# Optimization experiments

Measured on AMD Instinct MI355X. Metric: run time of the kernel, lower is better.

## Reference

```python
import jax, jax.numpy as jnp
import numpy as np

N_NODES = 100000
N_EDGES = 3200000
N_REL = 32
DIM = 64


def setup_inputs() -> dict:
    key = jax.random.key(0)
    ks = jax.random.split(key, 12)
    inp = {
        "ego_embeddings": jax.random.normal(ks[0], (N_NODES, DIM), dtype=jnp.float32),
        "rel_embeddings": jax.random.normal(ks[1], (N_REL, DIM), dtype=jnp.float32),
        "row_idx": jax.random.randint(ks[2], (N_EDGES,), 0, N_NODES, dtype=jnp.int32),
        "col_idx": jax.random.randint(ks[3], (N_EDGES,), 0, N_NODES, dtype=jnp.int32),
        "vals": jax.random.uniform(ks[4], (N_EDGES,), dtype=jnp.float32),
        "row_idx_r": jax.random.randint(ks[5], (N_EDGES,), 0, N_NODES, dtype=jnp.int32),
        "rel_idx": jax.random.randint(ks[6], (N_EDGES,), 0, N_REL, dtype=jnp.int32),
        "vals_r": jax.random.uniform(ks[7], (N_EDGES,), dtype=jnp.float32),
        "W1": jax.random.normal(ks[8], (DIM, DIM), dtype=jnp.float32) / np.sqrt(DIM),
        "b1": jnp.zeros((DIM,), dtype=jnp.float32),
        "W2": jax.random.normal(ks[9], (DIM, DIM), dtype=jnp.float32) / np.sqrt(DIM),
        "b2": jnp.zeros((DIM,), dtype=jnp.float32),
    }
    return inp


def _spmm(row, col, val, dense, num_rows):
    # sparse [num_rows, K] (COO) @ dense [K, D] -> [num_rows, D]
    msgs = val[:, None] * dense[col]  # [E, D]
    return jax.ops.segment_sum(msgs, row, num_segments=num_rows)


def reference(ego_embeddings, rel_embeddings, row_idx, col_idx, vals,
              row_idx_r, rel_idx, vals_r, W1, b1, W2, b2):
    n = ego_embeddings.shape[0]
    side = _spmm(row_idx, col_idx, vals, ego_embeddings, n) \
         + 0.1 * _spmm(row_idx_r, rel_idx, vals_r, rel_embeddings, n)
    # 'bi' aggregator
    add_emb = ego_embeddings + side
    sum_emb = jax.nn.leaky_relu(add_emb @ W1.T + b1, negative_slope=0.01)
    bi_emb = jax.nn.leaky_relu((ego_embeddings * side) @ W2.T + b2, negative_slope=0.01)
    # message dropout: identity in eval mode
    return bi_emb + sum_emb
```

## Files before the change

### kernel.cpp

```cpp
#include <hip/hip_runtime.h>
#include <hip/hip_fp16.h>

#define NN 100000
#define NE 3200000
#define NR 32
#define DIM 64
#define SCAN_BLK 1024
#define NBLK_SCAN ((NN + SCAN_BLK - 1) / SCAN_BLK)


__global__ __launch_bounds__(256) void hist_kernel(
    const int* __restrict__ row,
    const int* __restrict__ row_r, const int* __restrict__ rel_i,
    const float* __restrict__ vals_r,
    int* __restrict__ offsets, float* __restrict__ coeff)
{
    int e = blockIdx.x * 256 + threadIdx.x;
    if (e >= NE) return;
    atomicAdd(&offsets[row[e]], 1);
    atomicAdd(&coeff[row_r[e] * NR + rel_i[e]], vals_r[e]);
}

__global__ __launch_bounds__(SCAN_BLK) void scan1_kernel(
    int* __restrict__ offsets, int* __restrict__ bsums)
{
    __shared__ int s[SCAN_BLK];
    int tid = threadIdx.x;
    int i = blockIdx.x * SCAN_BLK + tid;
    int v = (i < NN) ? offsets[i] : 0;
    s[tid] = v;
    __syncthreads();
    for (int off = 1; off < SCAN_BLK; off <<= 1) {
        int t = (tid >= off) ? s[tid - off] : 0;
        __syncthreads();
        s[tid] += t;
        __syncthreads();
    }
    if (i < NN) offsets[i] = s[tid] - v;
    if (tid == SCAN_BLK - 1) bsums[blockIdx.x] = s[tid];
}

__global__ __launch_bounds__(128) void scan2_kernel(int* __restrict__ bsums)
{
    __shared__ int s[128];
    int tid = threadIdx.x;
    int v = (tid < NBLK_SCAN) ? bsums[tid] : 0;
    s[tid] = v;
    __syncthreads();
    for (int off = 1; off < 128; off <<= 1) {
        int t = (tid >= off) ? s[tid - off] : 0;
        __syncthreads();
        s[tid] += t;
        __syncthreads();
    }
    if (tid < NBLK_SCAN) bsums[tid] = s[tid] - v;
}

__global__ __launch_bounds__(SCAN_BLK) void scan3_kernel(
    int* __restrict__ offsets, const int* __restrict__ bsums)
{
    int i = blockIdx.x * SCAN_BLK + threadIdx.x;
    if (i < NN) offsets[i] += bsums[blockIdx.x];
}

__global__ __launch_bounds__(256) void scatter_kernel(
    const int* __restrict__ row, const int* __restrict__ col,
    const float* __restrict__ vals,
    int* __restrict__ offsets, int* __restrict__ ecol, __half* __restrict__ eval)
{
    int e = blockIdx.x * 256 + threadIdx.x;
    if (e >= NE) return;
    int pos = atomicAdd(&offsets[row[e]], 1);
    ecol[pos] = col[e];
    eval[pos] = __float2half(vals[e]);
}

__global__ __launch_bounds__(256) void gather_finalize_kernel(
    const float* __restrict__ ego, const float* __restrict__ rel_emb,
    const int* __restrict__ offsets, const int* __restrict__ ecol,
    const __half* __restrict__ eval, const float* __restrict__ coeff,
    const float* __restrict__ W1, const float* __restrict__ b1,
    const float* __restrict__ W2, const float* __restrict__ b2,
    float* __restrict__ out)
{
    __shared__ float sW1t[DIM * DIM];
    __shared__ float sW2t[DIM * DIM];
    __shared__ float sRel[NR * DIM];

    for (int i = threadIdx.x; i < DIM * DIM; i += 256) {
        int dd = i >> 6, kk = i & 63;
        sW1t[kk * DIM + dd] = W1[i];
        sW2t[kk * DIM + dd] = W2[i];
    }
    for (int i = threadIdx.x; i < NR * DIM; i += 256) sRel[i] = rel_emb[i];
    __syncthreads();

    const int wave = threadIdx.x >> 6;
    const int lane = threadIdx.x & 63;
    const int NPW  = 4;
    int node0 = (blockIdx.x * 4 + wave) * NPW;

    float bb1 = b1[lane];
    float bb2 = b2[lane];

    for (int t = 0; t < NPW; ++t) {
        int n = node0 + t;
        if (n >= NN) return;

        int start = (n > 0) ? offsets[n - 1] : 0;
        int end   = offsets[n];

        float acc = 0.0f;
        for (int base = start; base < end; base += 64) {
            int idx = base + lane;
            int   c = 0;
            float v = 0.0f;
            if (idx < end) { c = ecol[idx]; v = __half2float(eval[idx]); }
            int m = min(64, end - base);
            for (int j = 0; j < m; ++j) {
                int   cc = __shfl(c, j, 64);
                float vv = __shfl(v, j, 64);
                acc += vv * ego[cc * DIM + lane];
            }
        }

        float cv = (lane < NR) ? coeff[n * NR + lane] : 0.0f;
        float rp = 0.0f;
        #pragma unroll
        for (int r = 0; r < NR; ++r) {
            float c = __shfl(cv, r, 64);
            rp += c * sRel[r * DIM + lane];
        }
        float sd = acc + 0.1f * rp;

        float egod = ego[n * DIM + lane];
        float addv = egod + sd;
        float biv  = egod * sd;

        float acc1 = bb1;
        float acc2 = bb2;
        #pragma unroll
        for (int k = 0; k < DIM; ++k) {
            float a = __shfl(addv, k, 64);
            float b = __shfl(biv,  k, 64);
            acc1 += a * sW1t[k * DIM + lane];
            acc2 += b * sW2t[k * DIM + lane];
        }
        acc1 = acc1 > 0.0f ? acc1 : 0.01f * acc1;
        acc2 = acc2 > 0.0f ? acc2 : 0.01f * acc2;
        out[n * DIM + lane] = acc1 + acc2;
    }
}

extern "C" void kernel_launch(void* const* d_in, const int* in_sizes, int n_in,
                              void* d_out, int out_size, void* d_ws, size_t ws_size,
                              hipStream_t stream)
{
    const float* ego   = (const float*)d_in[0];
    const float* rel   = (const float*)d_in[1];
    const int*   row   = (const int*)  d_in[2];
    const int*   col   = (const int*)  d_in[3];
    const float* vals  = (const float*)d_in[4];
    const int*   row_r = (const int*)  d_in[5];
    const int*   rel_i = (const int*)  d_in[6];
    const float* vals_r= (const float*)d_in[7];
    const float* W1    = (const float*)d_in[8];
    const float* b1    = (const float*)d_in[9];
    const float* W2    = (const float*)d_in[10];
    const float* b2    = (const float*)d_in[11];
    float* out = (float*)d_out;

    int*    offsets = (int*)d_ws;
    int*    bsums   = offsets + NN;
    float*  coeff   = (float*)(bsums + 128);
    int*    ecol    = (int*)(coeff + (size_t)NN * NR);
    __half* eval    = (__half*)(ecol + NE);

    size_t zero_bytes = ((size_t)NN + 128 + (size_t)NN * NR) * sizeof(int);
    hipMemsetAsync(d_ws, 0, zero_bytes, stream);

    int eblocks = (NE + 255) / 256;
    hist_kernel<<<eblocks, 256, 0, stream>>>(row, row_r, rel_i, vals_r,
                                             offsets, coeff);
    scan1_kernel<<<NBLK_SCAN, SCAN_BLK, 0, stream>>>(offsets, bsums);
    scan2_kernel<<<1, 128, 0, stream>>>(bsums);
    scan3_kernel<<<NBLK_SCAN, SCAN_BLK, 0, stream>>>(offsets, bsums);
    scatter_kernel<<<eblocks, 256, 0, stream>>>(row, col, vals,
                                                offsets, ecol, eval);
    int gblocks = (NN + 15) / 16;
    gather_finalize_kernel<<<gblocks, 256, 0, stream>>>(
        ego, rel, offsets, ecol, eval, coeff, W1, b1, W2, b2, out);
}
```

Measured before the change: 1.104 ms.

## Pack CSR edges into 64-bit records and gather rows with float4 quarter-waves

The scatter stage now writes each edge as one 64-bit record holding the column index and the fp32 value, replacing separate int and half arrays. The gather loop assigns each 16-lane quarter-wave one edge, loading a full 256-byte ego row as float4. Each wave handles 8 edges per iteration, where before it processed one edge at a time after broadcasting indices through shuffles. Partial sums are then reduced across quarter-waves and redistributed per lane. This cuts serial shuffle overhead and raises memory-level parallelism, at the cost of wider edge records and a cross-lane reduction.

Result: faster. 986.6 us (-10.7%).

```diff
diff --git a/kernel.cpp b/kernel.cpp
--- a/kernel.cpp
+++ b/kernel.cpp
@@ -1,5 +1,4 @@
 #include <hip/hip_runtime.h>
-#include <hip/hip_fp16.h>
 
 #define NN 100000
 #define NE 3200000
@@ -7,6 +6,8 @@
 #define DIM 64
 #define SCAN_BLK 1024
 #define NBLK_SCAN ((NN + SCAN_BLK - 1) / SCAN_BLK)
+
+typedef unsigned long long u64;
 
 
 __global__ __launch_bounds__(256) void hist_kernel(
@@ -66,19 +67,19 @@
 __global__ __launch_bounds__(256) void scatter_kernel(
     const int* __restrict__ row, const int* __restrict__ col,
     const float* __restrict__ vals,
-    int* __restrict__ offsets, int* __restrict__ ecol, __half* __restrict__ eval)
+    int* __restrict__ offsets, u64* __restrict__ recs)
 {
     int e = blockIdx.x * 256 + threadIdx.x;
     if (e >= NE) return;
     int pos = atomicAdd(&offsets[row[e]], 1);
-    ecol[pos] = col[e];
-    eval[pos] = __float2half(vals[e]);
+    union { float f; unsigned u; } uv; uv.f = vals[e];
+    recs[pos] = ((u64)uv.u << 32) | (unsigned)(col[e]);
 }
 
 __global__ __launch_bounds__(256) void gather_finalize_kernel(
     const float* __restrict__ ego, const float* __restrict__ rel_emb,
-    const int* __restrict__ offsets, const int* __restrict__ ecol,
-    const __half* __restrict__ eval, const float* __restrict__ coeff,
+    const int* __restrict__ offsets, const u64* __restrict__ recs,
+    const float* __restrict__ coeff,
     const float* __restrict__ W1, const float* __restrict__ b1,
     const float* __restrict__ W2, const float* __restrict__ b2,
     float* __restrict__ out)
@@ -97,9 +98,12 @@
 
     const int wave = threadIdx.x >> 6;
     const int lane = threadIdx.x & 63;
-    const int NPW  = 4;
+    const int g = lane >> 4;
+    const int q = lane & 15;
+    const int NPW = 4;
     int node0 = (blockIdx.x * 4 + wave) * NPW;
 
+    const float4* ego4 = (const float4*)ego;
     float bb1 = b1[lane];
     float bb2 = b2[lane];
 
@@ -110,19 +114,54 @@
         int start = (n > 0) ? offsets[n - 1] : 0;
         int end   = offsets[n];
 
-        float acc = 0.0f;
-        for (int base = start; base < end; base += 64) {
-            int idx = base + lane;
-            int   c = 0;
-            float v = 0.0f;
-            if (idx < end) { c = ecol[idx]; v = __half2float(eval[idx]); }
-            int m = min(64, end - base);
-            for (int j = 0; j < m; ++j) {
-                int   cc = __shfl(c, j, 64);
-                float vv = __shfl(v, j, 64);
-                acc += vv * ego[cc * DIM + lane];
+        float4 acc0 = make_float4(0.f, 0.f, 0.f, 0.f);
+        float4 acc1 = make_float4(0.f, 0.f, 0.f, 0.f);
+
+        int e0 = start;
+        for (; e0 + 8 <= end; e0 += 8) {
+            u64 rA = recs[e0 + g];
+            u64 rB = recs[e0 + 4 + g];
+            int   cA = (int)(unsigned)rA;
+            float vA = __uint_as_float((unsigned)(rA >> 32));
+            int   cB = (int)(unsigned)rB;
+            float vB = __uint_as_float((unsigned)(rB >> 32));
+            float4 a = ego4[(size_t)cA * 16 + q];
+            float4 b = ego4[(size_t)cB * 16 + q];
+            acc0.x += vA * a.x; acc0.y += vA * a.y;
+            acc0.z += vA * a.z; acc0.w += vA * a.w;
+            acc1.x += vB * b.x; acc1.y += vB * b.y;
+            acc1.z += vB * b.z; acc1.w += vB * b.w;
+        }
+        for (; e0 < end; e0 += 4) {
+            int e = e0 + g;
+            if (e < end) {
+                u64 rA = recs[e];
+                int   cA = (int)(unsigned)rA;
+                float vA = __uint_as_float((unsigned)(rA >> 32));
+                float4 a = ego4[(size_t)cA * 16 + q];
+                acc0.x += vA * a.x; acc0.y += vA * a.y;
+                acc0.z += vA * a.z; acc0.w += vA * a.w;
             }
         }
+        acc0.x += acc1.x; acc0.y += acc1.y;
+        acc0.z += acc1.z; acc0.w += acc1.w;
+
+        acc0.x += __shfl_xor(acc0.x, 16, 64);
+        acc0.y += __shfl_xor(acc0.y, 16, 64);
+        acc0.z += __shfl_xor(acc0.z, 16, 64);
+        acc0.w += __shfl_xor(acc0.w, 16, 64);
+        acc0.x += __shfl_xor(acc0.x, 32, 64);
+        acc0.y += __shfl_xor(acc0.y, 32, 64);
+        acc0.z += __shfl_xor(acc0.z, 32, 64);
+        acc0.w += __shfl_xor(acc0.w, 32, 64);
+
+        int src = lane >> 2;
+        float sx = __shfl(acc0.x, src, 64);
+        float sy = __shfl(acc0.y, src, 64);
+        float sz = __shfl(acc0.z, src, 64);
+        float sw = __shfl(acc0.w, src, 64);
+        int cmp = lane & 3;
+        float sd = (cmp == 0) ? sx : (cmp == 1) ? sy : (cmp == 2) ? sz : sw;
 
         float cv = (lane < NR) ? coeff[n * NR + lane] : 0.0f;
         float rp = 0.0f;
@@ -131,24 +170,24 @@
             float c = __shfl(cv, r, 64);
             rp += c * sRel[r * DIM + lane];
         }
-        float sd = acc + 0.1f * rp;
+        sd += 0.1f * rp;
 
         float egod = ego[n * DIM + lane];
         float addv = egod + sd;
         float biv  = egod * sd;
 
-        float acc1 = bb1;
-        float acc2 = bb2;
+        float acc1s = bb1;
+        float acc2s = bb2;
         #pragma unroll
         for (int k = 0; k < DIM; ++k) {
             float a = __shfl(addv, k, 64);
             float b = __shfl(biv,  k, 64);
-            acc1 += a * sW1t[k * DIM + lane];
-            acc2 += b * sW2t[k * DIM + lane];
-        }
-        acc1 = acc1 > 0.0f ? acc1 : 0.01f * acc1;
-        acc2 = acc2 > 0.0f ? acc2 : 0.01f * acc2;
-        out[n * DIM + lane] = acc1 + acc2;
+            acc1s += a * sW1t[k * DIM + lane];
+            acc2s += b * sW2t[k * DIM + lane];
+        }
+        acc1s = acc1s > 0.0f ? acc1s : 0.01f * acc1s;
+        acc2s = acc2s > 0.0f ? acc2s : 0.01f * acc2s;
+        out[n * DIM + lane] = acc1s + acc2s;
     }
 }
 
@@ -170,11 +209,10 @@
     const float* b2    = (const float*)d_in[11];
     float* out = (float*)d_out;
 
-    int*    offsets = (int*)d_ws;
-    int*    bsums   = offsets + NN;
-    float*  coeff   = (float*)(bsums + 128);
-    int*    ecol    = (int*)(coeff + (size_t)NN * NR);
-    __half* eval    = (__half*)(ecol + NE);
+    int*   offsets = (int*)d_ws;
+    int*   bsums   = offsets + NN;
+    float* coeff   = (float*)(bsums + 128);
+    u64*   recs    = (u64*)(coeff + (size_t)NN * NR);
 
     size_t zero_bytes = ((size_t)NN + 128 + (size_t)NN * NR) * sizeof(int);
     hipMemsetAsync(d_ws, 0, zero_bytes, stream);
@@ -186,8 +224,8 @@
     scan2_kernel<<<1, 128, 0, stream>>>(bsums);
     scan3_kernel<<<NBLK_SCAN, SCAN_BLK, 0, stream>>>(offsets, bsums);
     scatter_kernel<<<eblocks, 256, 0, stream>>>(row, col, vals,
-                                                offsets, ecol, eval);
+                                                offsets, recs);
     int gblocks = (NN + 15) / 16;
     gather_finalize_kernel<<<gblocks, 256, 0, stream>>>(
-        ego, rel, offsets, ecol, eval, coeff, W1, b1, W2, b2, out);
-}
+        ego, rel, offsets, recs, coeff, W1, b1, W2, b2, out);
+}
```
